# Kernel optimization log

Measured on AMD Instinct MI355X. Metric: run time of the kernel, lower is better.

Reference implementation:

```python
import jax, jax.numpy as jnp
import numpy as np

NUM_ROUTING = 3  # init kwarg num_routing


def setup_inputs() -> dict:
    key = jax.random.key(0)
    k1, k2 = jax.random.split(key)
    # x: [B=128, N=1152 primary caps, C_in=8]
    x = jax.random.normal(k1, (128, 1152, 8), dtype=jnp.float32)
    # dc_w: [capsules_dim=10, num_capsules=1152, C_in=8, C_out=16]
    dc_w = jax.random.normal(k2, (10, 1152, 8, 16), dtype=jnp.float32)
    return {"x": x, "dc_w": dc_w}


def reference(x, dc_w):
    # u = x[None,:,:,None,:] @ dc_w[:,None,:,:,:]  -> [D, B, N, 1, C_out]
    u = jnp.einsum('bni,dnio->dbno', x, dc_w)[:, :, :, None, :]
    b = jnp.zeros_like(u)
    v = None
    for i in range(NUM_ROUTING):  # small fixed routing loop
        c = jax.nn.softmax(b, axis=2)                 # softmax over primary caps
        s = jnp.sum(c * u, axis=2, keepdims=True)     # [D, B, 1, 1, C_out]
        # faithful to source: norm is taken over the (singleton) axis 2,
        # so the squash coefficient is elementwise s^2 / ((1+s^2) * |s|)
        sq = s * s
        coeff = sq / ((1.0 + sq) * jnp.sqrt(sq))
        v = coeff * s
        if i != NUM_ROUTING - 1:
            b = b + jnp.sum(u * v, axis=-1, keepdims=True)  # agreement update
    return v  # [D, B, 1, 1, C_out]
```

## Files before the change

kernel.cpp:

```cpp
#include <hip/hip_runtime.h>
#include <hip/hip_bf16.h>
#include <math.h>

constexpr int NCAPS = 1152;
constexpr int CIN   = 8;
constexpr int COUT  = 16;
constexpr int BATCH = 128;
constexpr int DCAPS = 10;

__global__ __launch_bounds__(256, 1) void u_kernel(
    const float* __restrict__ x,
    const float* __restrict__ w,
    __hip_bfloat16* __restrict__ u)
{
    const int i  = blockIdx.x;
    const int bh = i & 1;
    const int nc = (i >> 1) % 72;
    const int d  = (i >> 1) / 72;

    const int t    = threadIdx.x;
    const int oq   = t & 3;
    const int bgrp = (t >> 2) & 3;
    const int nl   = t >> 4;
    const int n    = nc * 16 + nl;
    const int b0   = bh * 64 + bgrp * 16;

    const float* wr = w + ((size_t)(d * NCAPS + n)) * (CIN * COUT) + oq * 4;
    float4 W[CIN];
    #pragma unroll
    for (int ii = 0; ii < CIN; ++ii)
        W[ii] = *(const float4*)(wr + ii * COUT);

    const float* xp = x + ((size_t)b0 * NCAPS + n) * CIN;
    __hip_bfloat16* up = u + ((size_t)(d * BATCH + b0) * NCAPS + n) * COUT + oq * 4;

    #pragma unroll
    for (int bi = 0; bi < 16; ++bi) {
        const float4* xr = (const float4*)(xp + (size_t)bi * NCAPS * CIN);
        float4 xa = xr[0], xc = xr[1];
        float xs[CIN] = {xa.x, xa.y, xa.z, xa.w, xc.x, xc.y, xc.z, xc.w};
        float4 acc = {0.f, 0.f, 0.f, 0.f};
        #pragma unroll
        for (int ii = 0; ii < CIN; ++ii) {
            acc.x = fmaf(xs[ii], W[ii].x, acc.x);
            acc.y = fmaf(xs[ii], W[ii].y, acc.y);
            acc.z = fmaf(xs[ii], W[ii].z, acc.z);
            acc.w = fmaf(xs[ii], W[ii].w, acc.w);
        }
        union { unsigned short us[4]; uint2 v; } pk;
        pk.us[0] = __bfloat16_as_ushort(__float2bfloat16(acc.x));
        pk.us[1] = __bfloat16_as_ushort(__float2bfloat16(acc.y));
        pk.us[2] = __bfloat16_as_ushort(__float2bfloat16(acc.z));
        pk.us[3] = __bfloat16_as_ushort(__float2bfloat16(acc.w));
        *(uint2*)(up + (size_t)bi * NCAPS * COUT) = pk.v;
    }
}

constexpr int BNT  = 256;
constexpr int BWAV = BNT / 64;
constexpr int JPT  = 9;

__device__ __forceinline__ void unpack8(const uint4 pv, float* f) {
    f[0] = __uint_as_float(pv.x << 16);
    f[1] = __uint_as_float(pv.x & 0xffff0000u);
    f[2] = __uint_as_float(pv.y << 16);
    f[3] = __uint_as_float(pv.y & 0xffff0000u);
    f[4] = __uint_as_float(pv.z << 16);
    f[5] = __uint_as_float(pv.z & 0xffff0000u);
    f[6] = __uint_as_float(pv.w << 16);
    f[7] = __uint_as_float(pv.w & 0xffff0000u);
}

__global__ __launch_bounds__(BNT, 1) void routing_kernel(
    const __hip_bfloat16* __restrict__ u,
    float* __restrict__ out)
{
    __shared__ float red[BWAV][COUT];
    __shared__ float zred[BWAV];
    __shared__ float vsh[COUT];

    const int i = blockIdx.x;
    const int d = i >> 7;
    const int b = i & 127;

    const int t    = threadIdx.x;
    const int wave = t >> 6;
    const int lane = t & 63;
    const int oh   = t & 1;
    const int r    = t >> 1;

    const __hip_bfloat16* up =
        u + ((size_t)(d * BATCH + b) * NCAPS) * COUT + oh * 8;

    uint4 upk[JPT];
    #pragma unroll
    for (int j = 0; j < JPT; ++j)
        upk[j] = *(const uint4*)(up + (size_t)(j * 128 + r) * COUT);

    float bb[JPT];
    #pragma unroll
    for (int j = 0; j < JPT; ++j) bb[j] = 0.f;

    #pragma unroll
    for (int it = 0; it < 3; ++it) {
        float p8[8] = {0.f,0.f,0.f,0.f,0.f,0.f,0.f,0.f};
        float z = 0.f;
        if (it == 0) {
            #pragma unroll
            for (int j = 0; j < JPT; ++j) {
                float uf[8]; unpack8(upk[j], uf);
                #pragma unroll
                for (int k = 0; k < 8; ++k) p8[k] += uf[k];
            }
        } else {
            #pragma unroll
            for (int j = 0; j < JPT; ++j) {
                float e = __expf(bb[j] - 20.f);
                z += e;
                float uf[8]; unpack8(upk[j], uf);
                #pragma unroll
                for (int k = 0; k < 8; ++k) p8[k] = fmaf(e, uf[k], p8[k]);
            }
        }
        #pragma unroll
        for (int off = 2; off < 64; off <<= 1) {
            #pragma unroll
            for (int k = 0; k < 8; ++k) p8[k] += __shfl_xor(p8[k], off);
            if (it != 0) z += __shfl_xor(z, off);
        }
        if (lane < 2) {
            #pragma unroll
            for (int k = 0; k < 8; ++k) red[wave][oh * 8 + k] = p8[k];
            if (it != 0 && lane == 0) zred[wave] = z;
        }
        __syncthreads();

        if (t < COUT) {
            float s = red[0][t];
            #pragma unroll
            for (int wv = 1; wv < BWAV; ++wv) s += red[wv][t];
            float scale;
            if (it == 0) {
                scale = 1.f / (float)NCAPS;
            } else {
                float Z = zred[0];
                #pragma unroll
                for (int wv = 1; wv < BWAV; ++wv) Z += zred[wv];
                scale = 1.f / Z;
            }
            s *= scale;
            float v = s * fabsf(s) / (1.f + s * s);
            vsh[t] = v;
            if (it == 2)
                out[((size_t)d * BATCH + b) * COUT + t] = v;
        }
        __syncthreads();

        if (it < 2) {
            float vloc[8];
            #pragma unroll
            for (int k = 0; k < 8; ++k) vloc[k] = vsh[oh * 8 + k];
            #pragma unroll
            for (int j = 0; j < JPT; ++j) {
                float uf[8]; unpack8(upk[j], uf);
                float dv = 0.f;
                #pragma unroll
                for (int k = 0; k < 8; ++k) dv = fmaf(uf[k], vloc[k], dv);
                dv += __shfl_xor(dv, 1);
                bb[j] += dv;
            }
            __syncthreads();
        }
    }
}

extern "C" void kernel_launch(void* const* d_in, const int* in_sizes, int n_in,
                              void* d_out, int out_size, void* d_ws, size_t ws_size,
                              hipStream_t stream) {
    const float* x = (const float*)d_in[0];
    const float* w = (const float*)d_in[1];
    float* out = (float*)d_out;
    __hip_bfloat16* u = (__hip_bfloat16*)d_ws;

    u_kernel<<<DCAPS * 72 * 2, 256, 0, stream>>>(x, w, u);
    routing_kernel<<<DCAPS * BATCH, BNT, 0, stream>>>(u, out);
}
```

Before: 86.58 us.

## Fuse u computation into routing kernel to eliminate intermediate buffer

Computes the prediction vectors u directly in registers inside the routing kernel instead of writing them to a bf16 workspace from a separate kernel. This removes the large global write and re-read of u and one kernel launch. In exchange each block recomputes from x and its d-slice of w, relying on cache reuse of w across blocks, which are reordered to interleave d and share weights. Occupancy hint raised to allow more resident blocks.

```diff
diff --git a/kernel.cpp b/kernel.cpp
--- a/kernel.cpp
+++ b/kernel.cpp
@@ -8,53 +8,6 @@
 constexpr int BATCH = 128;
 constexpr int DCAPS = 10;
 
-__global__ __launch_bounds__(256, 1) void u_kernel(
-    const float* __restrict__ x,
-    const float* __restrict__ w,
-    __hip_bfloat16* __restrict__ u)
-{
-    const int i  = blockIdx.x;
-    const int bh = i & 1;
-    const int nc = (i >> 1) % 72;
-    const int d  = (i >> 1) / 72;
-
-    const int t    = threadIdx.x;
-    const int oq   = t & 3;
-    const int bgrp = (t >> 2) & 3;
-    const int nl   = t >> 4;
-    const int n    = nc * 16 + nl;
-    const int b0   = bh * 64 + bgrp * 16;
-
-    const float* wr = w + ((size_t)(d * NCAPS + n)) * (CIN * COUT) + oq * 4;
-    float4 W[CIN];
-    #pragma unroll
-    for (int ii = 0; ii < CIN; ++ii)
-        W[ii] = *(const float4*)(wr + ii * COUT);
-
-    const float* xp = x + ((size_t)b0 * NCAPS + n) * CIN;
-    __hip_bfloat16* up = u + ((size_t)(d * BATCH + b0) * NCAPS + n) * COUT + oq * 4;
-
-    #pragma unroll
-    for (int bi = 0; bi < 16; ++bi) {
-        const float4* xr = (const float4*)(xp + (size_t)bi * NCAPS * CIN);
-        float4 xa = xr[0], xc = xr[1];
-        float xs[CIN] = {xa.x, xa.y, xa.z, xa.w, xc.x, xc.y, xc.z, xc.w};
-        float4 acc = {0.f, 0.f, 0.f, 0.f};
-        #pragma unroll
-        for (int ii = 0; ii < CIN; ++ii) {
-            acc.x = fmaf(xs[ii], W[ii].x, acc.x);
-            acc.y = fmaf(xs[ii], W[ii].y, acc.y);
-            acc.z = fmaf(xs[ii], W[ii].z, acc.z);
-            acc.w = fmaf(xs[ii], W[ii].w, acc.w);
-        }
-        union { unsigned short us[4]; uint2 v; } pk;
-        pk.us[0] = __bfloat16_as_ushort(__float2bfloat16(acc.x));
-        pk.us[1] = __bfloat16_as_ushort(__float2bfloat16(acc.y));
-        pk.us[2] = __bfloat16_as_ushort(__float2bfloat16(acc.z));
-        pk.us[3] = __bfloat16_as_ushort(__float2bfloat16(acc.w));
-        *(uint2*)(up + (size_t)bi * NCAPS * COUT) = pk.v;
-    }
-}
 
 constexpr int BNT  = 256;
 constexpr int BWAV = BNT / 64;
@@ -71,8 +24,9 @@
     f[7] = __uint_as_float(pv.w & 0xffff0000u);
 }
 
-__global__ __launch_bounds__(BNT, 1) void routing_kernel(
-    const __hip_bfloat16* __restrict__ u,
+__global__ __launch_bounds__(BNT, 5) void fused_caps_kernel(
+    const float* __restrict__ x,
+    const float* __restrict__ w,
     float* __restrict__ out)
 {
     __shared__ float red[BWAV][COUT];
@@ -80,8 +34,9 @@
     __shared__ float vsh[COUT];
 
     const int i = blockIdx.x;
-    const int d = i >> 7;
-    const int b = i & 127;
+    int d, b;
+    if (i < 1024) { d = i & 7; b = i >> 3; }
+    else { const int j = i - 1024; d = 8 + (j & 1); b = j >> 1; }
 
     const int t    = threadIdx.x;
     const int wave = t >> 6;
@@ -89,13 +44,43 @@
     const int oh   = t & 1;
     const int r    = t >> 1;
 
-    const __hip_bfloat16* up =
-        u + ((size_t)(d * BATCH + b) * NCAPS) * COUT + oh * 8;
+    const float* xb = x + (size_t)b * (NCAPS * CIN);
+    const float* wd = w + (size_t)d * ((size_t)NCAPS * CIN * COUT) + oh * 8;
 
     uint4 upk[JPT];
     #pragma unroll
-    for (int j = 0; j < JPT; ++j)
-        upk[j] = *(const uint4*)(up + (size_t)(j * 128 + r) * COUT);
+    for (int j = 0; j < JPT; ++j) {
+        const int n = j * 128 + r;
+        const float4* xr = (const float4*)(xb + (size_t)n * CIN);
+        const float4 xa = xr[0], xc = xr[1];
+        const float xs[CIN] = {xa.x, xa.y, xa.z, xa.w, xc.x, xc.y, xc.z, xc.w};
+        const float* wr = wd + (size_t)n * (CIN * COUT);
+        float4 a0 = {0.f, 0.f, 0.f, 0.f};
+        float4 a1 = {0.f, 0.f, 0.f, 0.f};
+        #pragma unroll
+        for (int ii = 0; ii < CIN; ++ii) {
+            const float4 w0 = *(const float4*)(wr + ii * COUT);
+            const float4 w1 = *(const float4*)(wr + ii * COUT + 4);
+            a0.x = fmaf(xs[ii], w0.x, a0.x);
+            a0.y = fmaf(xs[ii], w0.y, a0.y);
+            a0.z = fmaf(xs[ii], w0.z, a0.z);
+            a0.w = fmaf(xs[ii], w0.w, a0.w);
+            a1.x = fmaf(xs[ii], w1.x, a1.x);
+            a1.y = fmaf(xs[ii], w1.y, a1.y);
+            a1.z = fmaf(xs[ii], w1.z, a1.z);
+            a1.w = fmaf(xs[ii], w1.w, a1.w);
+        }
+        union { unsigned short us[8]; uint4 v; } pk;
+        pk.us[0] = __bfloat16_as_ushort(__float2bfloat16(a0.x));
+        pk.us[1] = __bfloat16_as_ushort(__float2bfloat16(a0.y));
+        pk.us[2] = __bfloat16_as_ushort(__float2bfloat16(a0.z));
+        pk.us[3] = __bfloat16_as_ushort(__float2bfloat16(a0.w));
+        pk.us[4] = __bfloat16_as_ushort(__float2bfloat16(a1.x));
+        pk.us[5] = __bfloat16_as_ushort(__float2bfloat16(a1.y));
+        pk.us[6] = __bfloat16_as_ushort(__float2bfloat16(a1.z));
+        pk.us[7] = __bfloat16_as_ushort(__float2bfloat16(a1.w));
+        upk[j] = pk.v;
+    }
 
     float bb[JPT];
     #pragma unroll
@@ -180,8 +165,7 @@
     const float* x = (const float*)d_in[0];
     const float* w = (const float*)d_in[1];
     float* out = (float*)d_out;
-    __hip_bfloat16* u = (__hip_bfloat16*)d_ws;
+    (void)d_ws; (void)ws_size;
 
-    u_kernel<<<DCAPS * 72 * 2, 256, 0, stream>>>(x, w, u);
-    routing_kernel<<<DCAPS * BATCH, BNT, 0, stream>>>(u, out);
+    fused_caps_kernel<<<DCAPS * BATCH, BNT, 0, stream>>>(x, w, out);
 }
```

Measured after the change: 210.6 us. 2.43x slower.
